# Kernel tuning notes

Hardware: AMD Instinct MI355X
Metric: run time of the kernel (lower is better)

The kernel has to match this reference:

```python
import jax, jax.numpy as jnp
import numpy as np

B, S, IN_DIM, D, H, L, C = 8, 1024, 256, 1024, 16, 6, 10
DK = D // H
EPS = 1e-5


def setup_inputs() -> dict:
    key = jax.random.key(0)
    ks = iter(jax.random.split(key, 64))
    n = lambda shape, s=0.02: jax.random.normal(next(ks), shape, dtype=jnp.float32) * s
    inp = {
        'x': jax.random.normal(next(ks), (B, S, IN_DIM), dtype=jnp.float32),
        'emb_w': n((IN_DIM, D)), 'emb_b': jnp.zeros((D,), jnp.float32),
        'Wq': n((L, D, D)), 'bq': jnp.zeros((L, D), jnp.float32),
        'Wk': n((L, D, D)), 'bk': jnp.zeros((L, D), jnp.float32),
        'Wv': n((L, D, D)), 'bv': jnp.zeros((L, D), jnp.float32),
        'Wo': n((L, D, D)), 'bo': jnp.zeros((L, D), jnp.float32),
        'W1': n((L, D, 4 * D)), 'b1': jnp.zeros((L, 4 * D), jnp.float32),
        'W2': n((L, 4 * D, D)), 'b2': jnp.zeros((L, D), jnp.float32),
        'ln1_s': jnp.ones((L, D), jnp.float32), 'ln1_b': jnp.zeros((L, D), jnp.float32),
        'ln2_s': jnp.ones((L, D), jnp.float32), 'ln2_b': jnp.zeros((L, D), jnp.float32),
        'fc_w': n((D, C)), 'fc_b': jnp.zeros((C,), jnp.float32),
    }
    return inp


def _pos_encoding_rows(n_rows):
    # Faithful to the torch module: pe is [max_len,1,D]; pe[:x.size(0)] picks the
    # first `batch` positions and broadcasts over the sequence dim.
    pos = jnp.arange(n_rows, dtype=jnp.float32)[:, None]
    div = jnp.exp(jnp.arange(0, D, 2, dtype=jnp.float32) * (-np.log(10000.0) / D))
    pe = jnp.zeros((n_rows, D), jnp.float32)
    pe = pe.at[:, 0::2].set(jnp.sin(pos * div)).at[:, 1::2].set(jnp.cos(pos * div))
    return pe


def _layer_norm(x, scale, bias):
    mu = jnp.mean(x, axis=-1, keepdims=True)
    var = jnp.mean(jnp.square(x - mu), axis=-1, keepdims=True)
    return (x - mu) * jax.lax.rsqrt(var + EPS) * scale + bias


def reference(x, emb_w, emb_b, Wq, bq, Wk, bk, Wv, bv, Wo, bo,
              W1, b1, W2, b2, ln1_s, ln1_b, ln2_s, ln2_b, fc_w, fc_b):
    h = x @ emb_w + emb_b                              # [B,S,D]
    h = h + _pos_encoding_rows(B)[:, None, :]          # broadcast pe[:B] over seq
    scale = 1.0 / np.sqrt(DK)
    for i in range(L):
        def heads(y, W, b):
            return (y @ W + b).reshape(B, S, H, DK).transpose(0, 2, 1, 3)  # bhsd
        q = heads(h, Wq[i], bq[i])
        k = heads(h, Wk[i], bk[i])
        v = heads(h, Wv[i], bv[i])
        scores = jnp.einsum('bhqd,bhkd->bhqk', q, k) * scale
        p = jax.nn.softmax(scores, axis=-1)
        o = jnp.einsum('bhqk,bhkd->bhqd', p, v)
        o = o.transpose(0, 2, 1, 3).reshape(B, S, D)
        attn_out = o @ Wo[i] + bo[i]
        h = _layer_norm(h + attn_out, ln1_s[i], ln1_b[i])
        ff = jax.nn.relu(h @ W1[i] + b1[i]) @ W2[i] + b2[i]
        h = _layer_norm(h + ff, ln2_s[i], ln2_b[i])
    pooled = jnp.mean(h, axis=1)                       # [B,D]
    return pooled @ fc_w + fc_b                        # [B,C]
```

## Files before the change

kernel.cpp:

```cpp
#include <hip/hip_runtime.h>
#include <stdint.h>

#define B_   8
#define S_   1024
#define IND  256
#define D_   1024
#define H_   16
#define DKH  64
#define L_   6
#define FF   4096
#define NTOK (B_*S_)

typedef __bf16 bf16;
typedef __attribute__((ext_vector_type(4))) float  f32x4;
typedef __attribute__((ext_vector_type(8))) __bf16 bf16x8;
typedef __attribute__((ext_vector_type(4))) __bf16 bf16x4;
typedef __attribute__((ext_vector_type(2))) __bf16 bf16x2;

#define AS1 __attribute__((address_space(1)))
#define AS3 __attribute__((address_space(3)))

__device__ __forceinline__ void gload16(const void* g, void* l) {
  __builtin_amdgcn_global_load_lds((AS1 void*)(const_cast<void*>(g)), (AS3 void*)l, 16, 0, 0);
}

__global__ __launch_bounds__(256)
void k_trans(const float* __restrict__ in, bf16* __restrict__ out,
             int K, int N, long inStride, long outStride) {
  __shared__ float t[64][65];
  const float* inp = in + (long)blockIdx.z * inStride;
  bf16* outp = out + (long)blockIdx.z * outStride;
  const int n0 = blockIdx.x * 64, k0 = blockIdx.y * 64;
  const int r = threadIdx.x >> 4;
  const int c4 = (threadIdx.x & 15) * 4;
  #pragma unroll
  for (int j = 0; j < 64; j += 16) {
    f32x4 v = *(const f32x4*)(inp + (long)(k0 + r + j) * N + n0 + c4);
    #pragma unroll
    for (int i = 0; i < 4; ++i) t[r + j][c4 + i] = v[i];
  }
  __syncthreads();
  #pragma unroll
  for (int j = 0; j < 64; j += 16) {
    const int n = r + j;
    bf16x4 o;
    #pragma unroll
    for (int i = 0; i < 4; ++i) o[i] = (bf16)t[c4 + i][n];
    *(bf16x4*)(outp + (long)(n0 + n) * K + k0 + c4) = o;
  }
}

__global__ __launch_bounds__(256)
void k_f2b(const float* __restrict__ in, bf16* __restrict__ out) {
  const long i = ((long)blockIdx.x * 256 + threadIdx.x) * 4;
  f32x4 v = *(const f32x4*)(in + i);
  bf16x4 o;
  #pragma unroll
  for (int j = 0; j < 4; ++j) o[j] = (bf16)v[j];
  *(bf16x4*)(out + i) = o;
}

__global__ __launch_bounds__(256)
void k_pe(float* __restrict__ pe) {
  const int i = blockIdx.x * 256 + threadIdx.x;
  const int b = i >> 10, d = i & 1023;
  const float k2 = (float)(d & ~1);
  const float dv = __expf(k2 * (-9.210340371976184f / (float)D_));
  const float a = (float)b * dv;
  pe[i] = (d & 1) ? cosf(a) : sinf(a);
}

__global__ __launch_bounds__(256)
void k_packb(const float* __restrict__ bq, const float* __restrict__ bk,
             const float* __restrict__ bv, float* __restrict__ out) {
  const int i = blockIdx.x * 256 + threadIdx.x;
  const int l = i / 3072, j = i % 3072;
  const float* src = (j < 1024) ? bq : ((j < 2048) ? bk : bv);
  out[i] = src[l * 1024 + (j & 1023)];
}

template<int EPI>
__global__ __launch_bounds__(256)
void k_gemm(const bf16* __restrict__ A, const bf16* __restrict__ Bt,
            const float* __restrict__ bias,
            void* __restrict__ out0, void* __restrict__ out1,
            const float* __restrict__ pe,
            int M, int N, int K) {
  __shared__ __align__(16) bf16 sA[128 * 32];
  __shared__ __align__(16) bf16 sB[128 * 32];
  const int tid = threadIdx.x;
  const int lane = tid & 63, wv = tid >> 6;
  const int bx = blockIdx.x, by = blockIdx.y;
  const int wm = wv >> 1, wn = wv & 1;
  const int lg = lane >> 4, lc = lane & 15;
  const long arow0 = (long)by * 128;
  const long brow0 = (long)bx * 128;
  const int c0 = (wv * 2 + 0) * 64 + lane;
  const int c1 = (wv * 2 + 1) * 64 + lane;
  const int r0 = c0 >> 2, s0 = c0 & 3;
  const int r1 = c1 >> 2, s1 = c1 & 3;
  bf16* ldsA0 = sA + (wv * 2 + 0) * 512;
  bf16* ldsA1 = sA + (wv * 2 + 1) * 512;
  bf16* ldsB0 = sB + (wv * 2 + 0) * 512;
  bf16* ldsB1 = sB + (wv * 2 + 1) * 512;
  const bf16* Ab = A + arow0 * K;
  const bf16* Bb = Bt + brow0 * K;
  f32x4 acc[4][4] = {};
  const int kT = K >> 5;
  for (int kt = 0; kt < kT; ++kt) {
    const int k0 = kt << 5;
    gload16(Ab + (long)r0 * K + k0 + s0 * 8, ldsA0);
    gload16(Ab + (long)r1 * K + k0 + s1 * 8, ldsA1);
    gload16(Bb + (long)r0 * K + k0 + s0 * 8, ldsB0);
    gload16(Bb + (long)r1 * K + k0 + s1 * 8, ldsB1);
    __syncthreads();
    bf16x8 af[4], bfr[4];
    #pragma unroll
    for (int mr = 0; mr < 4; ++mr)
      af[mr] = *(const bf16x8*)(sA + (wm * 64 + mr * 16 + lc) * 32 + lg * 8);
    #pragma unroll
    for (int nc = 0; nc < 4; ++nc)
      bfr[nc] = *(const bf16x8*)(sB + (wn * 64 + nc * 16 + lc) * 32 + lg * 8);
    #pragma unroll
    for (int mr = 0; mr < 4; ++mr)
      #pragma unroll
      for (int nc = 0; nc < 4; ++nc)
        acc[mr][nc] = __builtin_amdgcn_mfma_f32_16x16x32_bf16(af[mr], bfr[nc], acc[mr][nc], 0, 0, 0);
    __syncthreads();
  }
  #pragma unroll
  for (int mr = 0; mr < 4; ++mr) {
    const int row0 = by * 128 + wm * 64 + mr * 16 + lg * 4;
    #pragma unroll
    for (int nc = 0; nc < 4; ++nc) {
      const int col = bx * 128 + wn * 64 + nc * 16 + lc;
      const float bvv = bias[col];
      #pragma unroll
      for (int r = 0; r < 4; ++r) {
        float v = acc[mr][nc][r] + bvv;
        const long rr = row0 + r;
        if constexpr (EPI == 0) {
          ((bf16*)out0)[rr * N + col] = (bf16)v;
        } else {
          const long bb = rr >> 10;
          v += pe[bb * D_ + col];
          ((bf16*)out1)[rr * N + col] = (bf16)v;
        }
      }
    }
  }
}

template<int EPI, int SPLIT>
__global__ __launch_bounds__(512, 2)
void k_gemm256(const bf16* __restrict__ A, const bf16* __restrict__ Bt,
               const float* __restrict__ bias,
               void* __restrict__ out0, void* __restrict__ out1,
               bf16* __restrict__ pout0, bf16* __restrict__ pout1,
               int M, int N, int K) {
  __shared__ __align__(16) bf16 lds[65536];
  const int tid = threadIdx.x;
  const int lane = tid & 63, wv = tid >> 6;
  const int wm = wv >> 2, wn = wv & 3;
  const int lg = lane >> 4, lc = lane & 15;
  const int gx = gridDim.x;
  const int nwg = gx * gridDim.y;
  int bid = blockIdx.x + blockIdx.y * gx;
  const int cpx = nwg >> 3;
  bid = (bid & 7) * cpx + (bid >> 3);
  const int bxs = bid % gx, bys = bid / gx;
  const int tileRow = bys * 256, tileCol = bxs * 256;
  const int kPart = SPLIT ? (K >> 1) : K;
  const long kOff = SPLIT ? (long)blockIdx.z * kPart : 0;
  const bf16* Abase = A + (long)tileRow * K + kOff;
  const bf16* Bbase = Bt + (long)tileCol * K + kOff;
  const long laneOff = (long)lc * K + lg * 8;
  f32x4 acc[8][4] = {};
  const int NT = kPart >> 6;
  const int NI = NT >> 1;

  auto stA = [&](int t, int h, int bb) {
    const int rg = h * 16 + wv * 2;
    const int mb = rg >> 1;
    const bf16* s = Abase + (long)(mb * 16) * K + t * 64 + laneOff;
    bf16* d = lds + bb * 32768 + rg * 512;
    gload16(s, d);
    gload16(s + 32, d + 512);
  };
  auto stB = [&](int t, int h, int bb) {
    const int rg = h * 16 + wv * 2;
    const int mb = rg >> 1;
    const bf16* s = Bbase + (long)(mb * 16) * K + t * 64 + laneOff;
    bf16* d = lds + bb * 32768 + 16384 + rg * 512;
    gload16(s, d);
    gload16(s + 32, d + 512);
  };

  bf16x8 aF[8];
  bf16x8 bF0[4], bF1[4];

#define LDA(BB, MH) do { _Pragma("unroll") for (int m = 0; m < 4; ++m) \
    _Pragma("unroll") for (int kk = 0; kk < 2; ++kk) \
      aF[m*2+kk] = *(const bf16x8*)(lds + (BB)*32768 + ((wm*8 + (MH)*4 + m)*2 + kk)*512 + lane*8); \
  } while(0)
#define LDB(BB, NH, DST) do { _Pragma("unroll") for (int n = 0; n < 2; ++n) \
    _Pragma("unroll") for (int kk = 0; kk < 2; ++kk) \
      DST[n*2+kk] = *(const bf16x8*)(lds + (BB)*32768 + 16384 + ((wn*4 + (NH)*2 + n)*2 + kk)*512 + lane*8); \
  } while(0)
#define MMA(MH, NH, BSRC) do { \
    __builtin_amdgcn_s_setprio(1); \
    _Pragma("unroll") for (int m = 0; m < 4; ++m) \
      _Pragma("unroll") for (int n = 0; n < 2; ++n) { \
        acc[(MH)*4+m][(NH)*2+n] = __builtin_amdgcn_mfma_f32_16x16x32_bf16(aF[m*2+0], BSRC[n*2+0], acc[(MH)*4+m][(NH)*2+n], 0, 0, 0); \
        acc[(MH)*4+m][(NH)*2+n] = __builtin_amdgcn_mfma_f32_16x16x32_bf16(aF[m*2+1], BSRC[n*2+1], acc[(MH)*4+m][(NH)*2+n], 0, 0, 0); \
      } \
    __builtin_amdgcn_s_setprio(0); \
  } while(0)
#define VM8 asm volatile("s_waitcnt vmcnt(8)" ::: "memory")
#define VM0 asm volatile("s_waitcnt vmcnt(0)" ::: "memory")
#define BAR __builtin_amdgcn_s_barrier()

  stA(0, 0, 0); stB(0, 0, 0); stA(0, 1, 0); stB(0, 1, 0);
  stA(1, 0, 1); stB(1, 0, 1); stA(1, 1, 1); stB(1, 1, 1);

  for (int i = 0; i < NI - 1; ++i) {
    const int t2 = 2 * i + 2, t3 = 2 * i + 3;
    VM8; BAR; LDA(0, 0); LDB(0, 0, bF0);   MMA(0, 0, bF0);
         BAR; LDB(0, 1, bF1); stA(t2, 0, 0);              MMA(0, 1, bF1);
         BAR; LDA(0, 1);      stB(t2, 0, 0);              MMA(1, 0, bF0);
         BAR; stA(t2, 1, 0);  stB(t2, 1, 0);              MMA(1, 1, bF1);
    VM8; BAR; LDA(1, 0); LDB(1, 0, bF0);   MMA(0, 0, bF0);
         BAR; LDB(1, 1, bF1); stA(t3, 0, 1);              MMA(0, 1, bF1);
         BAR; LDA(1, 1);      stB(t3, 0, 1);              MMA(1, 0, bF0);
         BAR; stA(t3, 1, 1);  stB(t3, 1, 1);              MMA(1, 1, bF1);
  }
  {
    VM8; BAR; LDA(0, 0); LDB(0, 0, bF0); MMA(0, 0, bF0);
         BAR; LDB(0, 1, bF1);            MMA(0, 1, bF1);
         BAR; LDA(0, 1);                 MMA(1, 0, bF0);
         BAR;                            MMA(1, 1, bF1);
    VM0; BAR; LDA(1, 0); LDB(1, 0, bF0); MMA(0, 0, bF0);
         BAR; LDB(1, 1, bF1);            MMA(0, 1, bF1);
         BAR; LDA(1, 1);                 MMA(1, 0, bF0);
         BAR;                            MMA(1, 1, bF1);
  }
#undef LDA
#undef LDB
#undef MMA
#undef VM8
#undef VM0
#undef BAR

  #pragma unroll
  for (int mr = 0; mr < 8; ++mr) {
    const int row0 = tileRow + wm * 128 + mr * 16 + lg * 4;
    #pragma unroll
    for (int nr = 0; nr < 4; ++nr) {
      const int col = tileCol + wn * 64 + nr * 16 + lc;
      if constexpr (SPLIT) {
        bf16* po = blockIdx.z ? pout1 : pout0;
        #pragma unroll
        for (int r = 0; r < 4; ++r)
          po[(long)(row0 + r) * N + col] = (bf16)acc[mr][nr][r];
      } else if constexpr (EPI == 2) {
        const float bvv = bias[col];
        const int which = col >> 10;
        const int hh = (col & 1023) >> 6;
        const int dk = col & 63;
        const long bb = row0 >> 10;
        const int sr = row0 & 1023;
        if (which == 2) {
          bf16x4 pk;
          #pragma unroll
          for (int r = 0; r < 4; ++r) pk[r] = (bf16)(acc[mr][nr][r] + bvv);
          *(bf16x4*)((bf16*)out1 + ((bb * H_ + hh) * (long)DKH + dk) * S_ + sr) = pk;
        } else {
          #pragma unroll
          for (int r = 0; r < 4; ++r) {
            float v = acc[mr][nr][r] + bvv;
            if (which == 0) v *= 0.125f;
            ((bf16*)out0)[(long)which * NTOK * D_ + ((bb * H_ + hh) * (long)S_ + sr + r) * DKH + dk] = (bf16)v;
          }
        }
      } else {
        const float bvv = bias[col];
        #pragma unroll
        for (int r = 0; r < 4; ++r) {
          float v = acc[mr][nr][r] + bvv;
          const long rr = row0 + r;
          if constexpr (EPI == 1) v = fmaxf(v, 0.f);
          ((bf16*)out0)[rr * N + col] = (bf16)v;
        }
      }
    }
  }
}

__global__ __launch_bounds__(256)
void k_flash(const bf16* __restrict__ qg, const bf16* __restrict__ kgl,
             const bf16* __restrict__ vtg, bf16* __restrict__ og) {
  __shared__ __align__(16) bf16 sK[64 * 64];
  __shared__ __align__(16) bf16 sV[64 * 64];
  __shared__ __align__(16) bf16 sP[4 * 16 * 64];
  const int tid = threadIdx.x, lane = tid & 63, wv = tid >> 6;
  const int lg = lane >> 4, lc = lane & 15;
  int bid = blockIdx.x + blockIdx.y * 16;
  bid = (bid & 7) * 256 + (bid >> 3);
  const int qt = bid & 15, bh = bid >> 4;
  const long base = (long)bh * S_ * DKH;
  const bf16* qb = qg + base;
  const bf16* kb = kgl + base;
  const bf16* vb = vtg + base;
  const int qrow = qt * 64 + wv * 16 + lc;
  const bf16x8 qf0 = *(const bf16x8*)(qb + (long)qrow * DKH + lg * 8);
  const bf16x8 qf1 = *(const bf16x8*)(qb + (long)qrow * DKH + 32 + lg * 8);
  float mrun = -3e38f, lrun = 0.f;
  f32x4 oacc[4] = {};
  bf16* sPw = sP + wv * (16 * 64);
  const int swzP = (lc & 7) << 4;
  const int c0 = wv * 128 + lane, c1 = c0 + 64;
  const int r0 = c0 >> 3, sl0 = (c0 & 7) ^ (r0 & 7);
  const int r1 = c1 >> 3, sl1 = (c1 & 7) ^ (r1 & 7);
  bf16* dst0 = sK + c0 * 8 - lane * 8;
  bf16* dst1 = sK + c1 * 8 - lane * 8;
  bf16* dstV0 = sV + c0 * 8 - lane * 8;
  bf16* dstV1 = sV + c1 * 8 - lane * 8;
  for (int kt = 0; kt < S_ / 64; ++kt) {
    const int gk = kt * 64;
    gload16(kb + (long)(gk + r0) * DKH + sl0 * 8, dst0);
    gload16(kb + (long)(gk + r1) * DKH + sl1 * 8, dst1);
    gload16(vb + (long)r0 * S_ + gk + sl0 * 8, dstV0);
    gload16(vb + (long)r1 * S_ + gk + sl1 * 8, dstV1);
    __syncthreads();
    f32x4 sacc[4] = {};
    #pragma unroll
    for (int nc = 0; nc < 4; ++nc) {
      const int kr = nc * 16 + lc;
      bf16x8 k0 = *(const bf16x8*)((char*)sK + kr * 128 + (((0 + lg) ^ (kr & 7)) << 4));
      bf16x8 k1 = *(const bf16x8*)((char*)sK + kr * 128 + (((4 + lg) ^ (kr & 7)) << 4));
      sacc[nc] = __builtin_amdgcn_mfma_f32_16x16x32_bf16(k0, qf0, sacc[nc], 0, 0, 0);
      sacc[nc] = __builtin_amdgcn_mfma_f32_16x16x32_bf16(k1, qf1, sacc[nc], 0, 0, 0);
    }
    float pm = sacc[0][0];
    #pragma unroll
    for (int nc = 0; nc < 4; ++nc)
      #pragma unroll
      for (int r = 0; r < 4; ++r) pm = fmaxf(pm, sacc[nc][r]);
    pm = fmaxf(pm, __shfl_xor(pm, 16));
    pm = fmaxf(pm, __shfl_xor(pm, 32));
    const float mnew = fmaxf(mrun, pm);
    const float fac = __expf(mrun - mnew);
    float ps = 0.f;
    #pragma unroll
    for (int nc = 0; nc < 4; ++nc)
      #pragma unroll
      for (int r = 0; r < 4; ++r) {
        const float p = __expf(sacc[nc][r] - mnew);
        sacc[nc][r] = p;
        ps += p;
      }
    ps += __shfl_xor(ps, 16);
    ps += __shfl_xor(ps, 32);
    lrun = lrun * fac + ps;
    mrun = mnew;
    #pragma unroll
    for (int nc = 0; nc < 4; ++nc)
      #pragma unroll
      for (int rp = 0; rp < 2; ++rp) {
        bf16x2 t;
        t[0] = (bf16)sacc[nc][rp * 2 + 0];
        t[1] = (bf16)sacc[nc][rp * 2 + 1];
        *(bf16x2*)((char*)sPw + lc * 128 + ((nc * 32 + lg * 8 + rp * 4) ^ swzP)) = t;
      }
    asm volatile("s_waitcnt lgkmcnt(0)" ::: "memory");
    __builtin_amdgcn_sched_barrier(0);
    float fr[4];
    #pragma unroll
    for (int r = 0; r < 4; ++r) fr[r] = __shfl(fac, lg * 4 + r);
    #pragma unroll
    for (int nc = 0; nc < 4; ++nc)
      #pragma unroll
      for (int r = 0; r < 4; ++r) oacc[nc][r] *= fr[r];
    #pragma unroll
    for (int m = 0; m < 2; ++m) {
      const bf16x8 pf = *(const bf16x8*)((char*)sPw + lc * 128 + ((m * 64 + lg * 16) ^ swzP));
      #pragma unroll
      for (int nc = 0; nc < 4; ++nc) {
        const int vr = nc * 16 + lc;
        bf16x8 vf = *(const bf16x8*)((char*)sV + vr * 128 + (((m * 4 + lg) ^ (vr & 7)) << 4));
        oacc[nc] = __builtin_amdgcn_mfma_f32_16x16x32_bf16(pf, vf, oacc[nc], 0, 0, 0);
      }
    }
    __syncthreads();
  }
  const int b = bh >> 4, h = bh & 15;
  const float linv = 1.f / lrun;
  #pragma unroll
  for (int r = 0; r < 4; ++r) {
    const float inv = __shfl(linv, lg * 4 + r);
    const int s = qt * 64 + wv * 16 + lg * 4 + r;
    const long obase = (((long)b * S_ + s) * H_ + h) * DKH;
    #pragma unroll
    for (int nc = 0; nc < 4; ++nc)
      og[obase + nc * 16 + lc] = (bf16)(oacc[nc][r] * inv);
  }
}

template<int TWO>
__global__ __launch_bounds__(256)
void k_addln(const bf16* __restrict__ hin, const bf16* __restrict__ dlt,
             const bf16* __restrict__ p0, const bf16* __restrict__ p1,
             const float* __restrict__ gb,
             const float* __restrict__ sc, const float* __restrict__ bi,
             bf16* __restrict__ hbout) {
  const int row = blockIdx.x, t = threadIdx.x;
  const long off = (long)row * D_ + t * 4;
  bf16x4 hv = *(const bf16x4*)(hin + off);
  f32x4 x;
  if constexpr (TWO) {
    bf16x4 a = *(const bf16x4*)(p0 + off);
    bf16x4 b = *(const bf16x4*)(p1 + off);
    f32x4 g = *(const f32x4*)(gb + t * 4);
    #pragma unroll
    for (int j = 0; j < 4; ++j) x[j] = (float)hv[j] + (float)a[j] + (float)b[j] + g[j];
  } else {
    bf16x4 dv = *(const bf16x4*)(dlt + off);
    #pragma unroll
    for (int j = 0; j < 4; ++j) x[j] = (float)hv[j] + (float)dv[j];
  }
  float s = 0.f, ss = 0.f;
  #pragma unroll
  for (int j = 0; j < 4; ++j) { s += x[j]; ss += x[j] * x[j]; }
  #pragma unroll
  for (int m = 1; m < 64; m <<= 1) { s += __shfl_xor(s, m); ss += __shfl_xor(ss, m); }
  __shared__ float red[8];
  const int w = t >> 6, ln = t & 63;
  if (ln == 0) { red[w] = s; red[4 + w] = ss; }
  __syncthreads();
  s = red[0] + red[1] + red[2] + red[3];
  ss = red[4] + red[5] + red[6] + red[7];
  const float mu = s * (1.f / D_);
  const float rstd = rsqrtf(ss * (1.f / D_) - mu * mu + 1e-5f);
  f32x4 scv = *(const f32x4*)(sc + t * 4);
  f32x4 biv = *(const f32x4*)(bi + t * 4);
  bf16x4 yb;
  #pragma unroll
  for (int j = 0; j < 4; ++j) yb[j] = (bf16)((x[j] - mu) * rstd * scv[j] + biv[j]);
  *(bf16x4*)(hbout + off) = yb;
}

__global__ __launch_bounds__(256)
void k_pool1(const bf16* __restrict__ h, float* __restrict__ part) {
  const int i = blockIdx.x * 256 + threadIdx.x;
  const int b = i >> 10, d = i & 1023;
  const int s0 = blockIdx.y * 128;
  float s = 0.f;
  for (int t = 0; t < 128; ++t) s += (float)h[((long)b * S_ + s0 + t) * D_ + d];
  part[(long)blockIdx.y * NTOK + i] = s;
}

__global__ __launch_bounds__(256)
void k_pool2(const float* __restrict__ part, float* __restrict__ pooled) {
  const int i = blockIdx.x * 256 + threadIdx.x;
  float s = 0.f;
  #pragma unroll
  for (int j = 0; j < 8; ++j) s += part[(long)j * NTOK + i];
  pooled[i] = s * (1.f / S_);
}

__global__ __launch_bounds__(64)
void k_fc(const float* __restrict__ pooled, const float* __restrict__ fw,
          const float* __restrict__ fb, float* __restrict__ out) {
  const int b = blockIdx.x / 10, c = blockIdx.x % 10;
  const int lane = threadIdx.x;
  float s = 0.f;
  for (int d = lane; d < D_; d += 64) s += pooled[b * D_ + d] * fw[d * 10 + c];
  #pragma unroll
  for (int m = 1; m < 64; m <<= 1) s += __shfl_xor(s, m);
  if (lane == 0) out[b * 10 + c] = s + fb[c];
}

extern "C" void kernel_launch(void* const* d_in, const int* in_sizes, int n_in,
                              void* d_out, int out_size, void* d_ws, size_t ws_size,
                              hipStream_t stream) {
  const float* x     = (const float*)d_in[0];
  const float* emb_w = (const float*)d_in[1];
  const float* emb_b = (const float*)d_in[2];
  const float* Wq    = (const float*)d_in[3];
  const float* bq    = (const float*)d_in[4];
  const float* Wk    = (const float*)d_in[5];
  const float* bk    = (const float*)d_in[6];
  const float* Wv    = (const float*)d_in[7];
  const float* bv    = (const float*)d_in[8];
  const float* Wo    = (const float*)d_in[9];
  const float* bo    = (const float*)d_in[10];
  const float* W1    = (const float*)d_in[11];
  const float* b1    = (const float*)d_in[12];
  const float* W2    = (const float*)d_in[13];
  const float* b2    = (const float*)d_in[14];
  const float* ln1s  = (const float*)d_in[15];
  const float* ln1b  = (const float*)d_in[16];
  const float* ln2s  = (const float*)d_in[17];
  const float* ln2b  = (const float*)d_in[18];
  const float* fcw   = (const float*)d_in[19];
  const float* fcb   = (const float*)d_in[20];

  char* w = (char*)d_ws;
  size_t off = 0;
  auto alloc = [&](size_t bytes) -> char* {
    char* p = w + off;
    off += (bytes + 255) & ~(size_t)255;
    return p;
  };
  bf16*  x_bf  = (bf16*) alloc((size_t)NTOK * IND * 2);
  bf16*  embT  = (bf16*) alloc((size_t)D_ * IND * 2);
  bf16*  qkvT  = (bf16*) alloc((size_t)L_ * 3 * D_ * D_ * 2);
  bf16*  woT   = (bf16*) alloc((size_t)L_ * D_ * D_ * 2);
  bf16*  w1T   = (bf16*) alloc((size_t)L_ * FF * D_ * 2);
  bf16*  w2T   = (bf16*) alloc((size_t)L_ * D_ * FF * 2);
  float* qkvB  = (float*)alloc((size_t)L_ * 3 * D_ * 4);
  float* pe    = (float*)alloc((size_t)B_ * D_ * 4);
  bf16*  h_b   = (bf16*) alloc((size_t)NTOK * D_ * 2);
  bf16*  delta = (bf16*) alloc((size_t)NTOK * D_ * 2);
  float* pooled= (float*)alloc((size_t)B_ * D_ * 4);
  float* part  = (float*)alloc((size_t)8 * NTOK * 4);
  bf16*  scratch = (bf16*)alloc((size_t)NTOK * FF * 2);
  bf16* qb  = scratch;
  bf16* kb  = scratch + (size_t)NTOK * D_;
  bf16* vTb = scratch + (size_t)2 * NTOK * D_;
  bf16* ob  = scratch + (size_t)3 * NTOK * D_;
  bf16* ffn1 = scratch;
  bf16* p0 = (bf16*)alloc((size_t)NTOK * D_ * 2);
  bf16* p1 = (bf16*)alloc((size_t)NTOK * D_ * 2);
  const bool canSplit = (off <= ws_size);
  (void)in_sizes; (void)n_in; (void)out_size;

  k_f2b<<<dim3(NTOK * IND / 1024), dim3(256), 0, stream>>>(x, x_bf);
  k_trans<<<dim3(D_ / 64, IND / 64, 1), dim3(256), 0, stream>>>(emb_w, embT, IND, D_, 0, 0);
  k_trans<<<dim3(D_ / 64, D_ / 64, L_), dim3(256), 0, stream>>>(Wq, qkvT,               D_, D_, (long)D_ * D_, (long)3 * D_ * D_);
  k_trans<<<dim3(D_ / 64, D_ / 64, L_), dim3(256), 0, stream>>>(Wk, qkvT + D_ * D_,     D_, D_, (long)D_ * D_, (long)3 * D_ * D_);
  k_trans<<<dim3(D_ / 64, D_ / 64, L_), dim3(256), 0, stream>>>(Wv, qkvT + 2 * D_ * D_, D_, D_, (long)D_ * D_, (long)3 * D_ * D_);
  k_trans<<<dim3(D_ / 64, D_ / 64, L_), dim3(256), 0, stream>>>(Wo, woT, D_, D_, (long)D_ * D_, (long)D_ * D_);
  k_trans<<<dim3(FF / 64, D_ / 64, L_), dim3(256), 0, stream>>>(W1, w1T, D_, FF, (long)D_ * FF, (long)FF * D_);
  k_trans<<<dim3(D_ / 64, FF / 64, L_), dim3(256), 0, stream>>>(W2, w2T, FF, D_, (long)FF * D_, (long)D_ * FF);
  k_pe<<<dim3(B_ * D_ / 256), dim3(256), 0, stream>>>(pe);
  k_packb<<<dim3(L_ * 3 * D_ / 256), dim3(256), 0, stream>>>(bq, bk, bv, qkvB);

  k_gemm<3><<<dim3(D_ / 128, NTOK / 128), dim3(256), 0, stream>>>(
      x_bf, embT, emb_b, nullptr, h_b, pe, NTOK, D_, IND);

  for (int l = 0; l < L_; ++l) {
    k_gemm256<2, 0><<<dim3(3 * D_ / 256, NTOK / 256), dim3(512), 0, stream>>>(
        h_b, qkvT + (size_t)l * 3 * D_ * D_, qkvB + l * 3 * D_,
        qb, vTb, nullptr, nullptr, NTOK, 3 * D_, D_);
    k_flash<<<dim3(S_ / 64, B_ * H_), dim3(256), 0, stream>>>(qb, kb, vTb, ob);
    if (canSplit) {
      k_gemm256<0, 1><<<dim3(D_ / 256, NTOK / 256, 2), dim3(512), 0, stream>>>(
          ob, woT + (size_t)l * D_ * D_, nullptr,
          nullptr, nullptr, p0, p1, NTOK, D_, D_);
      k_addln<1><<<dim3(NTOK), dim3(256), 0, stream>>>(
          h_b, nullptr, p0, p1, bo + l * D_, ln1s + l * D_, ln1b + l * D_, h_b);
    } else {
      k_gemm256<0, 0><<<dim3(D_ / 256, NTOK / 256), dim3(512), 0, stream>>>(
          ob, woT + (size_t)l * D_ * D_, bo + l * D_,
          delta, nullptr, nullptr, nullptr, NTOK, D_, D_);
      k_addln<0><<<dim3(NTOK), dim3(256), 0, stream>>>(
          h_b, delta, nullptr, nullptr, nullptr, ln1s + l * D_, ln1b + l * D_, h_b);
    }
    k_gemm256<1, 0><<<dim3(FF / 256, NTOK / 256), dim3(512), 0, stream>>>(
        h_b, w1T + (size_t)l * FF * D_, b1 + l * FF,
        ffn1, nullptr, nullptr, nullptr, NTOK, FF, D_);
    if (canSplit) {
      k_gemm256<0, 1><<<dim3(D_ / 256, NTOK / 256, 2), dim3(512), 0, stream>>>(
          ffn1, w2T + (size_t)l * D_ * FF, nullptr,
          nullptr, nullptr, p0, p1, NTOK, D_, FF);
      k_addln<1><<<dim3(NTOK), dim3(256), 0, stream>>>(
          h_b, nullptr, p0, p1, b2 + l * D_, ln2s + l * D_, ln2b + l * D_, h_b);
    } else {
      k_gemm256<0, 0><<<dim3(D_ / 256, NTOK / 256), dim3(512), 0, stream>>>(
          ffn1, w2T + (size_t)l * D_ * FF, b2 + l * D_,
          delta, nullptr, nullptr, nullptr, NTOK, D_, FF);
      k_addln<0><<<dim3(NTOK), dim3(256), 0, stream>>>(
          h_b, delta, nullptr, nullptr, nullptr, ln2s + l * D_, ln2b + l * D_, h_b);
    }
  }

  k_pool1<<<dim3(NTOK / 256, 8), dim3(256), 0, stream>>>(h_b, part);
  k_pool2<<<dim3(NTOK / 256), dim3(256), 0, stream>>>(part, pooled);
  k_fc<<<dim3(B_ * 10), dim3(64), 0, stream>>>(pooled, fcw, fcb, (float*)d_out);
}
```

Before: 2.180 ms.

## Add 8-phase pipelined 256x256 GEMM kernel for FFN1

Introduces a new GEMM kernel for the FFN up-projection. It splits each pair of K tiles into eight phases that interleave LDS fragment reads, async global-to-LDS loads and MFMA sub-blocks, with barriers and s_setprio to raise priority while the math runs. The aim is to hide memory latency behind the matrix cores. It adds tightly hand-tuned waitcnt logic and a 128KB LDS double buffer, and it assumes K is a multiple of 128.

```diff
diff --git a/kernel.cpp b/kernel.cpp
--- a/kernel.cpp
+++ b/kernel.cpp
@@ -296,6 +296,135 @@
   }
 }
 
+template<int EPI>
+__global__ __launch_bounds__(512, 2)
+void k_gemm8p(const bf16* __restrict__ A, const bf16* __restrict__ Bt,
+              const float* __restrict__ bias,
+              bf16* __restrict__ out0,
+              int M, int N, int K) {
+  __shared__ __align__(16) bf16 lds[65536];
+  const int tid = threadIdx.x;
+  const int lane = tid & 63, wv = tid >> 6;
+  const int wm = wv >> 2, wn = wv & 3;
+  const int lg = lane >> 4, lc = lane & 15;
+  const int gx = gridDim.x;
+  const int nwg = gx * gridDim.y;
+  int bid = blockIdx.x + blockIdx.y * gx;
+  const int cpx = nwg >> 3;
+  bid = (bid & 7) * cpx + (bid >> 3);
+  const int bxs = bid % gx, bys = bid / gx;
+  const int tileRow = bys * 256, tileCol = bxs * 256;
+  const bf16* Abase = A + (long)tileRow * K;
+  const bf16* Bbase = Bt + (long)tileCol * K;
+  const long laneOff = (long)lc * K + lg * 8;
+  f32x4 acc[8][4] = {};
+  const int NT = K >> 6;
+  const int NI = NT >> 1;
+
+  auto stA = [&](int t, int h, int bb) {
+    const int rg = h * 16 + wv * 2;
+    const int mb = rg >> 1;
+    const bf16* s = Abase + (long)(mb * 16) * K + t * 64 + laneOff;
+    bf16* d = lds + bb * 32768 + rg * 512;
+    gload16(s, d);
+    gload16(s + 32, d + 512);
+  };
+  auto stB = [&](int t, int h, int bb) {
+    const int rg = h * 16 + wv * 2;
+    const int mb = rg >> 1;
+    const bf16* s = Bbase + (long)(mb * 16) * K + t * 64 + laneOff;
+    bf16* d = lds + bb * 32768 + 16384 + rg * 512;
+    gload16(s, d);
+    gload16(s + 32, d + 512);
+  };
+
+  bf16x8 aF[8];
+  bf16x8 bF0[4], bF1[4];
+
+#define LDA(BB, MH) do { _Pragma("unroll") for (int m = 0; m < 4; ++m) \
+    _Pragma("unroll") for (int kk = 0; kk < 2; ++kk) \
+      aF[m*2+kk] = *(const bf16x8*)(lds + (BB)*32768 + ((wm*8 + (MH)*4 + m)*2 + kk)*512 + lane*8); \
+  } while(0)
+#define LDB(BB, NH, DST) do { _Pragma("unroll") for (int n = 0; n < 2; ++n) \
+    _Pragma("unroll") for (int kk = 0; kk < 2; ++kk) \
+      DST[n*2+kk] = *(const bf16x8*)(lds + (BB)*32768 + 16384 + ((wn*4 + (NH)*2 + n)*2 + kk)*512 + lane*8); \
+  } while(0)
+#define MMA(MH, NH, BSRC) do { \
+    _Pragma("unroll") for (int m = 0; m < 4; ++m) \
+      _Pragma("unroll") for (int n = 0; n < 2; ++n) { \
+        acc[(MH)*4+m][(NH)*2+n] = __builtin_amdgcn_mfma_f32_16x16x32_bf16(aF[m*2+0], BSRC[n*2+0], acc[(MH)*4+m][(NH)*2+n], 0, 0, 0); \
+        acc[(MH)*4+m][(NH)*2+n] = __builtin_amdgcn_mfma_f32_16x16x32_bf16(aF[m*2+1], BSRC[n*2+1], acc[(MH)*4+m][(NH)*2+n], 0, 0, 0); \
+      } \
+  } while(0)
+#define NOP (void)0
+#define VM4 asm volatile("s_waitcnt vmcnt(4)" ::: "memory")
+#define VM0 asm volatile("s_waitcnt vmcnt(0)" ::: "memory")
+#define PH(RD, ST, VM, MH, NH, BSRC) do { \
+    RD; ST; VM; \
+    __builtin_amdgcn_sched_barrier(0); \
+    __builtin_amdgcn_s_barrier(); \
+    asm volatile("s_waitcnt lgkmcnt(0)" ::: "memory"); \
+    __builtin_amdgcn_sched_barrier(0); \
+    __builtin_amdgcn_s_setprio(1); \
+    MMA(MH, NH, BSRC); \
+    __builtin_amdgcn_s_setprio(0); \
+    __builtin_amdgcn_s_barrier(); \
+  } while(0)
+
+  stB(0, 0, 0); stB(0, 1, 0); stA(0, 0, 0); stA(0, 1, 0);
+  stB(1, 0, 1); stB(1, 1, 1);
+  VM4;
+  __builtin_amdgcn_s_barrier();
+
+  for (int i = 0; i < NI - 1; ++i) {
+    const int t1 = 2 * i + 1, t2 = 2 * i + 2, t3 = 2 * i + 3;
+    PH(LDA(0, 0); LDB(0, 0, bF0), stA(t1, 0, 1), NOP, 0, 0, bF0);
+    PH(LDB(0, 1, bF1),            stA(t1, 1, 1), NOP, 0, 1, bF1);
+    PH(LDA(0, 1),                 stB(t2, 0, 0), NOP, 1, 0, bF0);
+    PH(NOP,                       stB(t2, 1, 0), VM4, 1, 1, bF1);
+    PH(LDA(1, 0); LDB(1, 0, bF0), stA(t2, 0, 0), NOP, 0, 0, bF0);
+    PH(LDB(1, 1, bF1),            stA(t2, 1, 0), NOP, 0, 1, bF1);
+    PH(LDA(1, 1),                 stB(t3, 0, 1), NOP, 1, 0, bF0);
+    PH(NOP,                       stB(t3, 1, 1), VM4, 1, 1, bF1);
+  }
+  {
+    const int tl = NT - 1;
+    PH(LDA(0, 0); LDB(0, 0, bF0), stA(tl, 0, 1), NOP, 0, 0, bF0);
+    PH(LDB(0, 1, bF1),            stA(tl, 1, 1), NOP, 0, 1, bF1);
+    PH(LDA(0, 1),                 NOP,           NOP, 1, 0, bF0);
+    PH(NOP,                       NOP,           VM0, 1, 1, bF1);
+    PH(LDA(1, 0); LDB(1, 0, bF0), NOP,           NOP, 0, 0, bF0);
+    PH(LDB(1, 1, bF1),            NOP,           NOP, 0, 1, bF1);
+    PH(LDA(1, 1),                 NOP,           NOP, 1, 0, bF0);
+    __builtin_amdgcn_s_setprio(1);
+    MMA(1, 1, bF1);
+    __builtin_amdgcn_s_setprio(0);
+  }
+#undef LDA
+#undef LDB
+#undef MMA
+#undef NOP
+#undef VM4
+#undef VM0
+#undef PH
+
+  #pragma unroll
+  for (int mr = 0; mr < 8; ++mr) {
+    const int row0 = tileRow + wm * 128 + mr * 16 + lg * 4;
+    #pragma unroll
+    for (int nr = 0; nr < 4; ++nr) {
+      const int col = tileCol + wn * 64 + nr * 16 + lc;
+      const float bvv = bias[col];
+      #pragma unroll
+      for (int r = 0; r < 4; ++r) {
+        float v = acc[mr][nr][r] + bvv;
+        if constexpr (EPI == 1) v = fmaxf(v, 0.f);
+        out0[(long)(row0 + r) * N + col] = (bf16)v;
+      }
+    }
+  }
+}
+
 __global__ __launch_bounds__(256)
 void k_flash(const bf16* __restrict__ qg, const bf16* __restrict__ kgl,
              const bf16* __restrict__ vtg, bf16* __restrict__ og) {
@@ -567,9 +696,9 @@
       k_addln<0><<<dim3(NTOK), dim3(256), 0, stream>>>(
           h_b, delta, nullptr, nullptr, nullptr, ln1s + l * D_, ln1b + l * D_, h_b);
     }
-    k_gemm256<1, 0><<<dim3(FF / 256, NTOK / 256), dim3(512), 0, stream>>>(
+    k_gemm8p<1><<<dim3(FF / 256, NTOK / 256), dim3(512), 0, stream>>>(
         h_b, w1T + (size_t)l * FF * D_, b1 + l * FF,
-        ffn1, nullptr, nullptr, nullptr, NTOK, FF, D_);
+        ffn1, NTOK, FF, D_);
     if (canSplit) {
       k_gemm256<0, 1><<<dim3(D_ / 256, NTOK / 256, 2), dim3(512), 0, stream>>>(
           ffn1, w2T + (size_t)l * D_ * FF, nullptr,
```

Measured after the change: 2.188 ms. Within noise of the previous version (+0.4%).

## Add 32x32x16 MFMA GEMM kernel with fused bias+ReLU for FFN1

Applied to the files above, without the earlier changes.

Adds a new 256x256-tile GEMM kernel that uses 32x32x16 bf16 MFMA instructions instead of the existing kernel's tiles. It double-buffers LDS through direct global-to-LDS loads, interleaves quarter-tile loads with MMA phases under barriers, and raises wave priority around the MFMA bursts. It is used only for the FFN1 projection, with bias and ReLU fused into its epilogue. The aim is higher matrix-core throughput and better overlap of loads with compute. The risks are heavy register pressure from 64 accumulator floats per fragment set, many barriers per k-step, and strided bf16 stores in the epilogue.

```diff
diff --git a/kernel.cpp b/kernel.cpp
--- a/kernel.cpp
+++ b/kernel.cpp
@@ -13,6 +13,7 @@
 
 typedef __bf16 bf16;
 typedef __attribute__((ext_vector_type(4))) float  f32x4;
+typedef __attribute__((ext_vector_type(16))) float f32x16;
 typedef __attribute__((ext_vector_type(8))) __bf16 bf16x8;
 typedef __attribute__((ext_vector_type(4))) __bf16 bf16x4;
 typedef __attribute__((ext_vector_type(2))) __bf16 bf16x2;
@@ -296,6 +297,122 @@
   }
 }
 
+__global__ __launch_bounds__(512, 2)
+void k_gemm32(const bf16* __restrict__ A, const bf16* __restrict__ Bt,
+              const float* __restrict__ bias,
+              bf16* __restrict__ out0,
+              int M, int N, int K) {
+  __shared__ __align__(16) bf16 lds[65536];
+  const int tid = threadIdx.x;
+  const int lane = tid & 63, wv = tid >> 6;
+  const int wm = wv >> 2, wn = wv & 3;
+  const int l31 = lane & 31, lh = lane >> 5;
+  const int gx = gridDim.x;
+  const int nwg = gx * gridDim.y;
+  int bid = blockIdx.x + blockIdx.y * gx;
+  const int cpx = nwg >> 3;
+  bid = (bid & 7) * cpx + (bid >> 3);
+  const int bxs = bid % gx, bys = bid / gx;
+  const int tileRow = bys * 256, tileCol = bxs * 256;
+  const bf16* Abase = A + (long)tileRow * K;
+  const bf16* Bbase = Bt + (long)tileCol * K;
+  const long laneOff = (long)l31 * K + lh * 8;
+  f32x16 acc[4][2] = {};
+  const int NT = K >> 6;
+  const int NI = NT >> 1;
+
+  auto stA = [&](int t, int h, int bb) {
+    #pragma unroll
+    for (int j = 0; j < 2; ++j) {
+      const int rg = h * 16 + wv * 2 + j;
+      const int mf = rg >> 2, ks = rg & 3;
+      const bf16* s = Abase + (long)(mf * 32) * K + t * 64 + ks * 16 + laneOff;
+      gload16(s, lds + bb * 32768 + rg * 512);
+    }
+  };
+  auto stB = [&](int t, int h, int bb) {
+    #pragma unroll
+    for (int j = 0; j < 2; ++j) {
+      const int rg = h * 16 + wv * 2 + j;
+      const int nf = rg >> 2, ks = rg & 3;
+      const bf16* s = Bbase + (long)(nf * 32) * K + t * 64 + ks * 16 + laneOff;
+      gload16(s, lds + bb * 32768 + 16384 + rg * 512);
+    }
+  };
+
+  bf16x8 aF[8];
+  bf16x8 bF0[4], bF1[4];
+
+#define LDA32(BB, MH) do { _Pragma("unroll") for (int j = 0; j < 2; ++j) \
+    _Pragma("unroll") for (int ks = 0; ks < 4; ++ks) { \
+      const int mf = wm * 4 + (MH) * 2 + j; \
+      aF[j*4+ks] = *(const bf16x8*)(lds + (BB)*32768 + (mf*4+ks)*512 + lane*8); \
+    } } while(0)
+#define LDB32(BB, NH, DST) do { const int nf = wn * 2 + (NH); \
+    _Pragma("unroll") for (int ks = 0; ks < 4; ++ks) \
+      DST[ks] = *(const bf16x8*)(lds + (BB)*32768 + 16384 + (nf*4+ks)*512 + lane*8); \
+  } while(0)
+#define MMA32(MH, NH, BSRC) do { \
+    __builtin_amdgcn_s_setprio(1); \
+    _Pragma("unroll") for (int j = 0; j < 2; ++j) \
+      _Pragma("unroll") for (int ks = 0; ks < 4; ++ks) \
+        acc[(MH)*2+j][NH] = __builtin_amdgcn_mfma_f32_32x32x16_bf16(aF[j*4+ks], BSRC[ks], acc[(MH)*2+j][NH], 0, 0, 0); \
+    __builtin_amdgcn_s_setprio(0); \
+  } while(0)
+#define VM8 asm volatile("s_waitcnt vmcnt(8)" ::: "memory")
+#define VM0 asm volatile("s_waitcnt vmcnt(0)" ::: "memory")
+#define BAR __builtin_amdgcn_s_barrier()
+
+  stA(0, 0, 0); stB(0, 0, 0); stA(0, 1, 0); stB(0, 1, 0);
+  stA(1, 0, 1); stB(1, 0, 1); stA(1, 1, 1); stB(1, 1, 1);
+
+  for (int i = 0; i < NI - 1; ++i) {
+    const int t2 = 2 * i + 2, t3 = 2 * i + 3;
+    VM8; BAR; LDA32(0, 0); LDB32(0, 0, bF0);   MMA32(0, 0, bF0);
+         BAR; LDB32(0, 1, bF1); stA(t2, 0, 0);              MMA32(0, 1, bF1);
+         BAR; LDA32(0, 1);      stB(t2, 0, 0);              MMA32(1, 0, bF0);
+         BAR; stA(t2, 1, 0);  stB(t2, 1, 0);                MMA32(1, 1, bF1);
+    VM8; BAR; LDA32(1, 0); LDB32(1, 0, bF0);   MMA32(0, 0, bF0);
+         BAR; LDB32(1, 1, bF1); stA(t3, 0, 1);              MMA32(0, 1, bF1);
+         BAR; LDA32(1, 1);      stB(t3, 0, 1);              MMA32(1, 0, bF0);
+         BAR; stA(t3, 1, 1);  stB(t3, 1, 1);                MMA32(1, 1, bF1);
+  }
+  {
+    VM8; BAR; LDA32(0, 0); LDB32(0, 0, bF0); MMA32(0, 0, bF0);
+         BAR; LDB32(0, 1, bF1);              MMA32(0, 1, bF1);
+         BAR; LDA32(0, 1);                   MMA32(1, 0, bF0);
+         BAR;                                MMA32(1, 1, bF1);
+    VM0; BAR; LDA32(1, 0); LDB32(1, 0, bF0); MMA32(0, 0, bF0);
+         BAR; LDB32(1, 1, bF1);              MMA32(0, 1, bF1);
+         BAR; LDA32(1, 1);                   MMA32(1, 0, bF0);
+         BAR;                                MMA32(1, 1, bF1);
+  }
+#undef LDA32
+#undef LDB32
+#undef MMA32
+#undef VM8
+#undef VM0
+#undef BAR
+
+  #pragma unroll
+  for (int mf = 0; mf < 4; ++mf) {
+    const int rowb = tileRow + wm * 128 + mf * 32 + lh * 4;
+    #pragma unroll
+    for (int nf = 0; nf < 2; ++nf) {
+      const int col = tileCol + wn * 64 + nf * 32 + l31;
+      const float bvv = bias[col];
+      #pragma unroll
+      for (int g = 0; g < 4; ++g)
+        #pragma unroll
+        for (int r = 0; r < 4; ++r) {
+          float v = acc[mf][nf][g * 4 + r] + bvv;
+          v = fmaxf(v, 0.f);
+          out0[(long)(rowb + g * 8 + r) * N + col] = (bf16)v;
+        }
+    }
+  }
+}
+
 __global__ __launch_bounds__(256)
 void k_flash(const bf16* __restrict__ qg, const bf16* __restrict__ kgl,
              const bf16* __restrict__ vtg, bf16* __restrict__ og) {
@@ -567,9 +684,9 @@
       k_addln<0><<<dim3(NTOK), dim3(256), 0, stream>>>(
           h_b, delta, nullptr, nullptr, nullptr, ln1s + l * D_, ln1b + l * D_, h_b);
     }
-    k_gemm256<1, 0><<<dim3(FF / 256, NTOK / 256), dim3(512), 0, stream>>>(
+    k_gemm32<<<dim3(FF / 256, NTOK / 256), dim3(512), 0, stream>>>(
         h_b, w1T + (size_t)l * FF * D_, b1 + l * FF,
-        ffn1, nullptr, nullptr, nullptr, NTOK, FF, D_);
+        ffn1, NTOK, FF, D_);
     if (canSplit) {
       k_gemm256<0, 1><<<dim3(D_ / 256, NTOK / 256, 2), dim3(512), 0, stream>>>(
           ffn1, w2T + (size_t)l * D_ * FF, nullptr,
```

Result: no change. 2.178 ms (-0.1%).
